# Kernel tuning notes

Measured on AMD Instinct MI355X. Metric: run time of the kernel, lower is better.

Reference implementation:

```python
import jax, jax.numpy as jnp
import numpy as np

B, L, D, H = 4, 2048, 1024, 16
HD = D // H

def setup_inputs() -> dict:
    key = jax.random.key(0)
    ks = jax.random.split(key, 11)
    s = 1.0 / np.sqrt(D)
    return {
        "query": jax.random.normal(ks[0], (B, L, D), jnp.float32),
        "key": jax.random.normal(ks[1], (B, L, D), jnp.float32),
        "value": jax.random.normal(ks[2], (B, L, D), jnp.float32),
        "Wq": jax.random.normal(ks[3], (D, D), jnp.float32) * s,
        "bq": jnp.zeros((D,), jnp.float32),
        "Wk": jax.random.normal(ks[4], (D, D), jnp.float32) * s,
        "bk": jnp.zeros((D,), jnp.float32),
        "Wv": jax.random.normal(ks[5], (D, D), jnp.float32) * s,
        "bv": jnp.zeros((D,), jnp.float32),
        "Wo": jax.random.normal(ks[6], (D, D), jnp.float32) * s,
        "bo": jnp.zeros((D,), jnp.float32),
    }

def reference(query, key, value, Wq, bq, Wk, bk, Wv, bv, Wo, bo):
    b = query.shape[0]
    # linear projections (torch Linear: x @ W.T + b)
    Q = query @ Wq.T + bq
    K = key @ Wk.T + bk
    V = value @ Wv.T + bv
    # split heads -> [b, h, l, hd]
    Q = Q.reshape(b, -1, H, HD).transpose(0, 2, 1, 3)
    K = K.reshape(b, -1, H, HD).transpose(0, 2, 1, 3)
    V = V.reshape(b, -1, H, HD).transpose(0, 2, 1, 3)
    energy = jnp.einsum('bhqd,bhkd->bhqk', Q, K) / jnp.sqrt(jnp.float32(HD))
    attn = jax.nn.softmax(energy, axis=-1)
    x = jnp.einsum('bhqk,bhkd->bhqd', attn, V)
    x = x.transpose(0, 2, 1, 3).reshape(b, -1, D)
    return x @ Wo.T + bo
```

## Files before the change

kernel.cpp:

```cpp
#include <hip/hip_runtime.h>

typedef float floatx4 __attribute__((ext_vector_type(4)));
typedef short bf16x8 __attribute__((ext_vector_type(8)));
typedef const unsigned int __attribute__((address_space(1))) gas_u32;
typedef unsigned int __attribute__((address_space(3))) las_u32;

#if __has_builtin(__builtin_amdgcn_exp2f)
#define EXP2F(x) __builtin_amdgcn_exp2f(x)
#else
#define EXP2F(x) exp2f(x)
#endif

__device__ __forceinline__ unsigned short f2bf(float x) {
    unsigned int u = __float_as_uint(x);
    unsigned int r = u + 0x7fffu + ((u >> 16) & 1u);
    return (unsigned short)(r >> 16);
}

__device__ __forceinline__ unsigned int pack2bf_t(float lo, float hi) {
    return (__float_as_uint(lo) >> 16) | (__float_as_uint(hi) & 0xffff0000u);
}

__device__ __forceinline__ void g2l16(const void* g, void* l) {
    __builtin_amdgcn_global_load_lds((gas_u32*)(unsigned long long)g,
                                     (las_u32*)(unsigned int)(unsigned long long)l,
                                     16, 0, 0);
}

__global__ __launch_bounds__(256) void cvt5_kernel(
    const float* __restrict__ k, const float* __restrict__ v,
    const float* __restrict__ wq, const float* __restrict__ wk, const float* __restrict__ wv,
    unsigned short* __restrict__ kb, unsigned short* __restrict__ vb,
    unsigned short* __restrict__ wqb, unsigned short* __restrict__ wkb,
    unsigned short* __restrict__ wvb) {
    const int ty = blockIdx.y;
    const float* src; unsigned short* dst; int n4;
    switch (ty) {
        case 0: src = k;  dst = kb;  n4 = 2097152; break;
        case 1: src = v;  dst = vb;  n4 = 2097152; break;
        case 2: src = wq; dst = wqb; n4 = 262144;  break;
        case 3: src = wk; dst = wkb; n4 = 262144;  break;
        default: src = wv; dst = wvb; n4 = 262144; break;
    }
    int i = blockIdx.x * 256 + threadIdx.x;
    if (i >= n4) return;
    float4 x = ((const float4*)src)[i];
    ushort4 o;
    o.x = f2bf(x.x); o.y = f2bf(x.y); o.z = f2bf(x.z); o.w = f2bf(x.w);
    ((ushort4*)dst)[i] = o;
}

__global__ __launch_bounds__(256) void cvt1_kernel(const float* __restrict__ wo,
                                                   unsigned short* __restrict__ wob) {
    int i = blockIdx.x * 256 + threadIdx.x;
    float4 x = ((const float4*)wo)[i];
    ushort4 o;
    o.x = f2bf(x.x); o.y = f2bf(x.y); o.z = f2bf(x.z); o.w = f2bf(x.w);
    ((ushort4*)wob)[i] = o;
}

template <int OUT_MODE, bool A_FP32>
__device__ __forceinline__ void gemm_body(const void* __restrict__ Aptr,
                                          const unsigned short* __restrict__ W,
                                          const float* __restrict__ bias,
                                          void* __restrict__ Cout,
                                          unsigned short* As, unsigned short* Bs,
                                          int m0, int n0, int N, int K, float scale) {
    const int t = threadIdx.x;
    const int lane = t & 63, w = t >> 6;
    const int lr = lane & 15, quad = lane >> 4;
    const int wm = (w & 1) * 64, wn = (w >> 1) * 64;

    const int s0 = w * 128 + lane, s1 = s0 + 64;
    const int r0 = s0 >> 2, c0 = ((s0 & 3) ^ (r0 & 3)) * 8;
    const int r1 = s1 >> 2, c1 = ((s1 & 3) ^ (r1 & 3)) * 8;
    const unsigned short* gw0 = W + (size_t)(n0 + r0) * K + c0;
    const unsigned short* gw1 = W + (size_t)(n0 + r1) * K + c1;
    unsigned short* lB0 = &Bs[(size_t)(w * 128) * 8];
    unsigned short* lB1 = &Bs[(size_t)(w * 128 + 64) * 8];

    const unsigned short* ga0 = nullptr;
    const unsigned short* ga1 = nullptr;
    unsigned short* lA0 = &As[(size_t)(w * 128) * 8];
    unsigned short* lA1 = &As[(size_t)(w * 128 + 64) * 8];
    if constexpr (!A_FP32) {
        const unsigned short* A = (const unsigned short*)Aptr;
        ga0 = A + (size_t)(m0 + r0) * K + c0;
        ga1 = A + (size_t)(m0 + r1) * K + c1;
    }

    floatx4 acc[4][4];
#pragma unroll
    for (int i = 0; i < 4; ++i)
#pragma unroll
        for (int j = 0; j < 4; ++j) acc[i][j] = (floatx4){0.f, 0.f, 0.f, 0.f};

    const int xs = (lr & 3);

    for (int k0 = 0; k0 < K; k0 += 32) {
        g2l16(gw0 + k0, lB0);
        g2l16(gw1 + k0, lB1);
        if constexpr (A_FP32) {
            const float* A = (const float*)Aptr;
#pragma unroll
            for (int i = 0; i < 4; ++i) {
                int idx = t + 256 * i;
                int row = idx >> 3;
                int c4 = (idx & 7) * 4;
                float4 v = *(const float4*)(A + (size_t)(m0 + row) * K + k0 + c4);
                ushort4 bv;
                bv.x = f2bf(v.x); bv.y = f2bf(v.y); bv.z = f2bf(v.z); bv.w = f2bf(v.w);
                *(ushort4*)&As[row * 32 + c4] = bv;
            }
        } else {
            g2l16(ga0 + k0, lA0);
            g2l16(ga1 + k0, lA1);
        }
        __syncthreads();

        bf16x8 af[4], bfr[4];
#pragma unroll
        for (int i = 0; i < 4; ++i) {
            int ch = A_FP32 ? quad : (quad ^ xs);
            af[i] = *(const bf16x8*)&As[(wm + i * 16 + lr) * 32 + ch * 8];
        }
#pragma unroll
        for (int j = 0; j < 4; ++j)
            bfr[j] = *(const bf16x8*)&Bs[(wn + j * 16 + lr) * 32 + ((quad ^ xs) * 8)];
#pragma unroll
        for (int i = 0; i < 4; ++i)
#pragma unroll
            for (int j = 0; j < 4; ++j) {
                if constexpr (OUT_MODE == 2)
                    acc[i][j] = __builtin_amdgcn_mfma_f32_16x16x32_bf16(bfr[j], af[i], acc[i][j], 0, 0, 0);
                else
                    acc[i][j] = __builtin_amdgcn_mfma_f32_16x16x32_bf16(af[i], bfr[j], acc[i][j], 0, 0, 0);
            }
        __syncthreads();
    }

    if constexpr (OUT_MODE == 2) {
        const int b = m0 >> 11;
        unsigned short* VT = (unsigned short*)Cout;
#pragma unroll
        for (int i = 0; i < 4; ++i) {
#pragma unroll
            for (int j = 0; j < 4; ++j) {
#pragma unroll
                for (int r = 0; r < 4; ++r) {
                    int d = n0 + wn + j * 16 + quad * 4 + r;
                    int tok = (m0 & 2047) + wm + i * 16 + lr;
                    float val = acc[i][j][r] + bias[d];
                    int t6 = tok & 63;
                    int ntok = (tok & ~63) | ((((t6 >> 3) ^ (d & 7)) << 3)) | (t6 & 7);
                    VT[(((size_t)b * 16 + (d >> 6)) * 64 + (d & 63)) * 2048 + ntok] = f2bf(val);
                }
            }
        }
    } else if constexpr (OUT_MODE == 3) {
        unsigned short* C = (unsigned short*)Cout;
#pragma unroll
        for (int i = 0; i < 4; ++i) {
#pragma unroll
            for (int j = 0; j < 4; ++j) {
#pragma unroll
                for (int r = 0; r < 4; ++r) {
                    int row = m0 + wm + i * 16 + quad * 4 + r;
                    int col = n0 + wn + j * 16 + lr;
                    float val = acc[i][j][r] + bias[col];
                    int r6 = row & 63;
                    int srow = (r6 & 32) | (((r6 >> 2) & 1) << 4) |
                               (((r6 >> 3) & 3) << 2) | (r6 & 3);
                    int nrow = (row & ~63) | srow;
                    int c6 = col & 63;
                    int ncol = (col & ~63) | ((((c6 >> 3) ^ (srow & 7)) << 3)) | (c6 & 7);
                    C[(size_t)nrow * N + ncol] = f2bf(val);
                }
            }
        }
    } else {
#pragma unroll
        for (int i = 0; i < 4; ++i) {
#pragma unroll
            for (int j = 0; j < 4; ++j) {
#pragma unroll
                for (int r = 0; r < 4; ++r) {
                    int row = m0 + wm + i * 16 + quad * 4 + r;
                    int col = n0 + wn + j * 16 + lr;
                    float val = (acc[i][j][r] + bias[col]) * scale;
                    if constexpr (OUT_MODE == 1)
                        ((unsigned short*)Cout)[(size_t)row * N + col] = f2bf(val);
                    else
                        ((float*)Cout)[(size_t)row * N + col] = val;
                }
            }
        }
    }
}

__device__ __forceinline__ void gemm_swz(int bx, int by, int& m0, int& n0) {
    const int hw = bx + 8 * by;
    const int wid = (hw & 7) * 64 + (hw >> 3);
    m0 = (wid >> 3) * 128;
    n0 = (wid & 7) * 128;
}

__global__ __launch_bounds__(256) void gemm_qkv(
    const float* __restrict__ query, const unsigned short* __restrict__ wqb,
    const float* __restrict__ bq, unsigned short* __restrict__ Qp,
    const unsigned short* __restrict__ kb, const unsigned short* __restrict__ wkb,
    const float* __restrict__ bk, unsigned short* __restrict__ Kp,
    const unsigned short* __restrict__ vb, const unsigned short* __restrict__ wvb,
    const float* __restrict__ bv, unsigned short* __restrict__ VTp, float qscale) {
    __shared__ unsigned short As[128 * 32];
    __shared__ unsigned short Bs[128 * 32];
    int m0, n0;
    gemm_swz(blockIdx.x, blockIdx.y, m0, n0);
    if (blockIdx.z == 0)
        gemm_body<1, true>(query, wqb, bq, Qp, As, Bs, m0, n0, 1024, 1024, qscale);
    else if (blockIdx.z == 1)
        gemm_body<3, false>(kb, wkb, bk, Kp, As, Bs, m0, n0, 1024, 1024, 1.0f);
    else
        gemm_body<2, false>(vb, wvb, bv, VTp, As, Bs, m0, n0, 1024, 1024, 1.0f);
}

__global__ __launch_bounds__(256) void gemm_o(const unsigned short* __restrict__ A,
                                              const unsigned short* __restrict__ W,
                                              const float* __restrict__ bias,
                                              void* __restrict__ C) {
    __shared__ unsigned short As[128 * 32];
    __shared__ unsigned short Bs[128 * 32];
    int m0, n0;
    gemm_swz(blockIdx.x, blockIdx.y, m0, n0);
    gemm_body<0, false>(A, W, bias, C, As, Bs, m0, n0, 1024, 1024, 1.0f);
}

__global__ __launch_bounds__(256) void attn_kernel(const unsigned short* __restrict__ Qp,
                                                   const unsigned short* __restrict__ Kp,
                                                   const unsigned short* __restrict__ VTp,
                                                   unsigned short* __restrict__ Xp) {
    constexpr int L = 2048, D = 1024;
    __shared__ unsigned short Ks[2][64 * 64];
    __shared__ unsigned short Vt[2][64 * 64];

    const int t = threadIdx.x;
    const int hw = blockIdx.x + 16 * blockIdx.y + 256 * blockIdx.z;
    const int wid = (hw & 7) * 128 + (hw >> 3);
    const int q0 = (wid & 15) * 128;
    const int h = (wid >> 4) & 15;
    const int b = wid >> 8;
    const int lane = t & 63;
    const int w = t >> 6;
    const int lr = lane & 15;
    const int quad = lane >> 4;
    const int x7 = lr & 7;

    const size_t kbase = ((size_t)(b * L)) * D + (size_t)h * 64;
    const size_t vtbase = ((size_t)(b * 16 + h)) * 64 * 2048;

    auto stage_async = [&](int buf, int kb2) {
        int k0 = kb2 * 64;
#pragma unroll
        for (int i = 0; i < 2; ++i) {
            int idx = t + 256 * i;
            int row = idx >> 3, c16 = idx & 7;
            g2l16(Kp + kbase + (size_t)(k0 + row) * D + c16 * 8,
                  &Ks[buf][(w * 64 + i * 256) * 8]);
            g2l16(VTp + vtbase + (size_t)row * 2048 + k0 + c16 * 8,
                  &Vt[buf][(w * 64 + i * 256) * 8]);
        }
    };

    stage_async(0, 0);

    const size_t qbase = ((size_t)(b * L + q0)) * D + (size_t)h * 64;
    bf16x8 bq[2][2];
#pragma unroll
    for (int qs = 0; qs < 2; ++qs)
#pragma unroll
        for (int s2 = 0; s2 < 2; ++s2)
            bq[qs][s2] = *(const bf16x8*)(Qp + qbase + (size_t)(w * 32 + qs * 16 + lr) * D +
                                          s2 * 32 + quad * 8);

    floatx4 o[2][4], ol[2];
#pragma unroll
    for (int qs = 0; qs < 2; ++qs) {
        ol[qs] = (floatx4){0.f, 0.f, 0.f, 0.f};
#pragma unroll
        for (int dt = 0; dt < 4; ++dt) o[qs][dt] = (floatx4){0.f, 0.f, 0.f, 0.f};
    }
    bf16x8 ones;
#pragma unroll
    for (int e = 0; e < 8; ++e) ones[e] = (short)0x3F80;

    __syncthreads();
    int cur = 0;

    const int kc0 = (quad ^ x7) * 8;
    const int kc1 = ((quad + 4) ^ x7) * 8;

    for (int kb = 0; kb < L / 64; ++kb) {
        if (kb < L / 64 - 1) stage_async(cur ^ 1, kb + 1);

        __builtin_amdgcn_s_setprio(1);
#pragma unroll
        for (int g = 0; g < 2; ++g) {
            bf16x8 akA0 = *(const bf16x8*)&Ks[cur][(g * 32 + lr) * 64 + kc0];
            bf16x8 akA1 = *(const bf16x8*)&Ks[cur][(g * 32 + lr) * 64 + kc1];
            bf16x8 akB0 = *(const bf16x8*)&Ks[cur][(g * 32 + 16 + lr) * 64 + kc0];
            bf16x8 akB1 = *(const bf16x8*)&Ks[cur][(g * 32 + 16 + lr) * 64 + kc1];
            bf16x8 vf[4];
#pragma unroll
            for (int dt = 0; dt < 4; ++dt)
                vf[dt] = *(const bf16x8*)&Vt[cur][(dt * 16 + lr) * 64 +
                                                  (((g * 4 + quad) ^ x7) * 8)];

            const floatx4 z4 = (floatx4){0.f, 0.f, 0.f, 0.f};
#pragma unroll
            for (int qs = 0; qs < 2; ++qs) {
                floatx4 stA = __builtin_amdgcn_mfma_f32_16x16x32_bf16(akA0, bq[qs][0], z4, 0, 0, 0);
                stA = __builtin_amdgcn_mfma_f32_16x16x32_bf16(akA1, bq[qs][1], stA, 0, 0, 0);
                floatx4 stB = __builtin_amdgcn_mfma_f32_16x16x32_bf16(akB0, bq[qs][0], z4, 0, 0, 0);
                stB = __builtin_amdgcn_mfma_f32_16x16x32_bf16(akB1, bq[qs][1], stB, 0, 0, 0);

                union { unsigned int u[4]; bf16x8 v; } pf;
                pf.u[0] = pack2bf_t(EXP2F(stA[0]), EXP2F(stA[1]));
                pf.u[1] = pack2bf_t(EXP2F(stA[2]), EXP2F(stA[3]));
                pf.u[2] = pack2bf_t(EXP2F(stB[0]), EXP2F(stB[1]));
                pf.u[3] = pack2bf_t(EXP2F(stB[2]), EXP2F(stB[3]));

                ol[qs] = __builtin_amdgcn_mfma_f32_16x16x32_bf16(pf.v, ones, ol[qs], 0, 0, 0);
#pragma unroll
                for (int dt = 0; dt < 4; ++dt)
                    o[qs][dt] = __builtin_amdgcn_mfma_f32_16x16x32_bf16(pf.v, vf[dt],
                                                                        o[qs][dt], 0, 0, 0);
            }
        }
        __builtin_amdgcn_s_setprio(0);

        if (kb < L / 64 - 1) {
            __syncthreads();
            cur ^= 1;
        }
    }

#pragma unroll
    for (int qs = 0; qs < 2; ++qs) {
#pragma unroll
        for (int r = 0; r < 4; ++r) {
            float inv = 1.0f / ol[qs][r];
            int q = q0 + w * 32 + qs * 16 + quad * 4 + r;
            size_t base = ((size_t)(b * L + q)) * D + (size_t)h * 64;
#pragma unroll
            for (int dt = 0; dt < 4; ++dt)
                Xp[base + dt * 16 + lr] = f2bf(o[qs][dt][r] * inv);
        }
    }
}

extern "C" void kernel_launch(void* const* d_in, const int* in_sizes, int n_in,
                              void* d_out, int out_size, void* d_ws, size_t ws_size,
                              hipStream_t stream) {
    const float* query = (const float*)d_in[0];
    const float* key_  = (const float*)d_in[1];
    const float* value = (const float*)d_in[2];
    const float* Wq = (const float*)d_in[3];
    const float* bq = (const float*)d_in[4];
    const float* Wk = (const float*)d_in[5];
    const float* bk = (const float*)d_in[6];
    const float* Wv = (const float*)d_in[7];
    const float* bv = (const float*)d_in[8];
    const float* Wo = (const float*)d_in[9];
    const float* bo = (const float*)d_in[10];
    float* out = (float*)d_out;

    const size_t MB16 = (size_t)8 * 1024 * 1024;

    unsigned short* Qp  = (unsigned short*)d_ws;
    unsigned short* kb  = Qp + MB16;
    unsigned short* vb  = kb + MB16;
    unsigned short* VTp = vb + MB16;
    unsigned short* Xp  = kb;
    unsigned short* wob = vb;
    unsigned short* Kp  = (unsigned short*)d_out;
    unsigned short* wqb = Kp + MB16;
    unsigned short* wkb = wqb + 1024 * 1024;
    unsigned short* wvb = wkb + 1024 * 1024;

    const float qscale = 0.125f * 1.44269504f;

    dim3 bb(256);
    cvt5_kernel<<<dim3(8192, 5), bb, 0, stream>>>(key_, value, Wq, Wk, Wv,
                                                  kb, vb, wqb, wkb, wvb);
    gemm_qkv<<<dim3(8, 64, 3), bb, 0, stream>>>(query, wqb, bq, Qp,
                                                kb, wkb, bk, Kp,
                                                vb, wvb, bv, VTp, qscale);
    attn_kernel<<<dim3(16, 16, 4), bb, 0, stream>>>(Qp, Kp, VTp, Xp);
    cvt1_kernel<<<dim3(1024), bb, 0, stream>>>(Wo, wob);
    gemm_o<<<dim3(8, 64), bb, 0, stream>>>(Xp, wob, bo, out);
}
```

Baseline: 348.7 us.

## Double-buffer GEMM LDS tiles to overlap global loads with MFMA compute

Splits the GEMM K-loop into stage and compute phases over two LDS buffers. The loads for the next K tile are issued before computing on the current one, with one barrier per tile instead of two. This is meant to hide global-to-LDS latency in the QKV and output projections. It doubles shared memory per block, which could lower occupancy.

Measured after the change: 345.5 us. No clear change (-0.9%).

```diff
diff --git a/kernel.cpp b/kernel.cpp
--- a/kernel.cpp
+++ b/kernel.cpp
@@ -76,13 +76,9 @@
     const int r1 = s1 >> 2, c1 = ((s1 & 3) ^ (r1 & 3)) * 8;
     const unsigned short* gw0 = W + (size_t)(n0 + r0) * K + c0;
     const unsigned short* gw1 = W + (size_t)(n0 + r1) * K + c1;
-    unsigned short* lB0 = &Bs[(size_t)(w * 128) * 8];
-    unsigned short* lB1 = &Bs[(size_t)(w * 128 + 64) * 8];
 
     const unsigned short* ga0 = nullptr;
     const unsigned short* ga1 = nullptr;
-    unsigned short* lA0 = &As[(size_t)(w * 128) * 8];
-    unsigned short* lA1 = &As[(size_t)(w * 128 + 64) * 8];
     if constexpr (!A_FP32) {
         const unsigned short* A = (const unsigned short*)Aptr;
         ga0 = A + (size_t)(m0 + r0) * K + c0;
@@ -97,36 +93,49 @@
 
     const int xs = (lr & 3);
 
-    for (int k0 = 0; k0 < K; k0 += 32) {
-        g2l16(gw0 + k0, lB0);
-        g2l16(gw1 + k0, lB1);
+    auto stage = [&](int buf, int k0) {
+        unsigned short* Ab = As + buf * 4096;
+        unsigned short* Bb = Bs + buf * 4096;
+        g2l16(gw0 + k0, &Bb[(size_t)(w * 128) * 8]);
+        g2l16(gw1 + k0, &Bb[(size_t)(w * 128 + 64) * 8]);
         if constexpr (A_FP32) {
             const float* A = (const float*)Aptr;
+            float4 v[4];
 #pragma unroll
             for (int i = 0; i < 4; ++i) {
                 int idx = t + 256 * i;
                 int row = idx >> 3;
                 int c4 = (idx & 7) * 4;
-                float4 v = *(const float4*)(A + (size_t)(m0 + row) * K + k0 + c4);
+                v[i] = *(const float4*)(A + (size_t)(m0 + row) * K + k0 + c4);
+            }
+#pragma unroll
+            for (int i = 0; i < 4; ++i) {
+                int idx = t + 256 * i;
+                int row = idx >> 3;
+                int c4 = (idx & 7) * 4;
                 ushort4 bv;
-                bv.x = f2bf(v.x); bv.y = f2bf(v.y); bv.z = f2bf(v.z); bv.w = f2bf(v.w);
-                *(ushort4*)&As[row * 32 + c4] = bv;
+                bv.x = f2bf(v[i].x); bv.y = f2bf(v[i].y);
+                bv.z = f2bf(v[i].z); bv.w = f2bf(v[i].w);
+                *(ushort4*)&Ab[row * 32 + c4] = bv;
             }
         } else {
-            g2l16(ga0 + k0, lA0);
-            g2l16(ga1 + k0, lA1);
-        }
-        __syncthreads();
-
+            g2l16(ga0 + k0, &Ab[(size_t)(w * 128) * 8]);
+            g2l16(ga1 + k0, &Ab[(size_t)(w * 128 + 64) * 8]);
+        }
+    };
+
+    auto compute = [&](int buf) {
+        const unsigned short* Ab = As + buf * 4096;
+        const unsigned short* Bb = Bs + buf * 4096;
         bf16x8 af[4], bfr[4];
 #pragma unroll
         for (int i = 0; i < 4; ++i) {
             int ch = A_FP32 ? quad : (quad ^ xs);
-            af[i] = *(const bf16x8*)&As[(wm + i * 16 + lr) * 32 + ch * 8];
+            af[i] = *(const bf16x8*)&Ab[(wm + i * 16 + lr) * 32 + ch * 8];
         }
 #pragma unroll
         for (int j = 0; j < 4; ++j)
-            bfr[j] = *(const bf16x8*)&Bs[(wn + j * 16 + lr) * 32 + ((quad ^ xs) * 8)];
+            bfr[j] = *(const bf16x8*)&Bb[(wn + j * 16 + lr) * 32 + ((quad ^ xs) * 8)];
 #pragma unroll
         for (int i = 0; i < 4; ++i)
 #pragma unroll
@@ -136,8 +145,22 @@
                 else
                     acc[i][j] = __builtin_amdgcn_mfma_f32_16x16x32_bf16(af[i], bfr[j], acc[i][j], 0, 0, 0);
             }
+    };
+
+    stage(0, 0);
+    __syncthreads();
+    for (int k0 = 0; k0 < K - 64; k0 += 64) {
+        stage(1, k0 + 32);
+        compute(0);
         __syncthreads();
-    }
+        stage(0, k0 + 64);
+        compute(1);
+        __syncthreads();
+    }
+    stage(1, K - 32);
+    compute(0);
+    __syncthreads();
+    compute(1);
 
     if constexpr (OUT_MODE == 2) {
         const int b = m0 >> 11;
@@ -212,8 +235,8 @@
     const float* __restrict__ bk, unsigned short* __restrict__ Kp,
     const unsigned short* __restrict__ vb, const unsigned short* __restrict__ wvb,
     const float* __restrict__ bv, unsigned short* __restrict__ VTp, float qscale) {
-    __shared__ unsigned short As[128 * 32];
-    __shared__ unsigned short Bs[128 * 32];
+    __shared__ unsigned short As[2 * 128 * 32];
+    __shared__ unsigned short Bs[2 * 128 * 32];
     int m0, n0;
     gemm_swz(blockIdx.x, blockIdx.y, m0, n0);
     if (blockIdx.z == 0)
@@ -228,8 +251,8 @@
                                               const unsigned short* __restrict__ W,
                                               const float* __restrict__ bias,
                                               void* __restrict__ C) {
-    __shared__ unsigned short As[128 * 32];
-    __shared__ unsigned short Bs[128 * 32];
+    __shared__ unsigned short As[2 * 128 * 32];
+    __shared__ unsigned short Bs[2 * 128 * 32];
     int m0, n0;
     gemm_swz(blockIdx.x, blockIdx.y, m0, n0);
     gemm_body<0, false>(A, W, bias, C, As, Bs, m0, n0, 1024, 1024, 1.0f);
```
